# Performance work log

Measured on AMD Instinct MI355X. Metric: run time of the kernel, lower is better.

The kernel has to match this reference:

```python
import math
import jax, jax.numpy as jnp
import numpy as np

B, A, M, NC = 32, 8400, 32, 80
TOP_K, ALPHA, BETA, EPS = 13, 1.0, 6.0, 1e-9
IMG = 640.0


def _ciou(b1, b2, eps=1e-7):
    # b1, b2 broadcastable [..., 4]; CIoU as in compute_iou (box1=gt, box2=pred)
    b1x1, b1y1, b1x2, b1y2 = b1[..., 0], b1[..., 1], b1[..., 2], b1[..., 3]
    b2x1, b2y1, b2x2, b2y2 = b2[..., 0], b2[..., 1], b2[..., 2], b2[..., 3]
    w1, h1 = b1x2 - b1x1, b1y2 - b1y1 + eps
    w2, h2 = b2x2 - b2x1, b2y2 - b2y1 + eps
    inter = (jnp.minimum(b1x2, b2x2) - jnp.maximum(b1x1, b2x1)).clip(0) * \
            (jnp.minimum(b1y2, b2y2) - jnp.maximum(b1y1, b2y1)).clip(0)
    union = w1 * h1 + w2 * h2 - inter + eps
    iou = inter / union
    cw = jnp.maximum(b1x2, b2x2) - jnp.minimum(b1x1, b2x1)
    ch = jnp.maximum(b1y2, b2y2) - jnp.minimum(b1y1, b2y1)
    c2 = cw ** 2 + ch ** 2 + eps
    rho2 = ((b2x1 + b2x2 - b1x1 - b1x2) ** 2 + (b2y1 + b2y2 - b1y1 - b1y2) ** 2) / 4.0
    v = (4.0 / math.pi ** 2) * (jnp.arctan(w2 / h2) - jnp.arctan(w1 / h1)) ** 2
    alpha = jax.lax.stop_gradient(v / (v - iou + (1.0 + eps)))
    return iou - (rho2 / c2 + v * alpha)


def setup_inputs() -> dict:
    key = jax.random.key(0)
    ks = jax.random.split(key, 8)
    pd_scores = jax.random.uniform(ks[0], (B, A, NC), jnp.float32)
    anc_points = jax.random.uniform(ks[1], (A, 2), jnp.float32) * IMG
    # predicted boxes around anchor points (valid x1<x2, y1<y2)
    off = jax.random.uniform(ks[2], (B, A, 4), jnp.float32) * 80.0 + 2.0
    pd_bboxes = jnp.concatenate([anc_points[None] - off[..., :2],
                                 anc_points[None] + off[..., 2:]], -1)
    # GT boxes: random centers and sizes, clipped to image
    c = jax.random.uniform(ks[3], (B, M, 2), jnp.float32) * IMG
    wh = jax.random.uniform(ks[4], (B, M, 2), jnp.float32) * 180.0 + 20.0
    gt_bboxes = jnp.concatenate([(c - wh / 2).clip(0, IMG), (c + wh / 2).clip(0, IMG)], -1)
    gt_labels = jax.random.randint(ks[5], (B, M, 1), 0, NC, jnp.int64)
    n_valid = jax.random.randint(ks[6], (B,), 1, M + 1)
    mask_gt = (jnp.arange(M)[None, :] < n_valid[:, None]).astype(jnp.float32)[..., None]
    return {"pd_scores": pd_scores, "pd_bboxes": pd_bboxes, "anc_points": anc_points,
            "gt_labels": gt_labels, "gt_bboxes": gt_bboxes, "mask_gt": mask_gt}


def reference(pd_scores, pd_bboxes, anc_points, gt_labels, gt_bboxes, mask_gt):
    b, a, nc = pd_scores.shape
    m = gt_bboxes.shape[1]
    dtype = pd_scores.dtype

    # anchors-inside-GT mask: [B,M,A]
    lt = gt_bboxes[:, :, None, :2]          # [B,M,1,2]
    rb = gt_bboxes[:, :, None, 2:]
    deltas = jnp.concatenate([anc_points[None, None] - lt,
                              rb - anc_points[None, None]], -1)  # [B,M,A,4]
    mask_in_gts = deltas.min(-1) > EPS
    mg = mask_gt[..., 0] > 0                 # [B,M] bool
    gt_mask = mask_in_gts & mg[:, :, None]

    # per-GT class score gather: pd_scores[b, :, gt_labels[b,m]] -> [B,M,A]
    labels = gt_labels[..., 0]               # [B,M]
    idx = jnp.broadcast_to(labels[:, :, None, None], (b, m, a, 1))
    gathered = jnp.take_along_axis(jnp.broadcast_to(pd_scores[:, None], (b, m, a, nc)), idx, axis=3)[..., 0]
    bbox_scores = jnp.where(gt_mask, gathered, 0.0)

    # CIoU overlaps (dense, masked) [B,M,A]
    iou = _ciou(gt_bboxes[:, :, None, :], pd_bboxes[:, None, :, :])
    overlaps = jnp.where(gt_mask, jnp.maximum(iou, 0.0), 0.0)

    align_metric = bbox_scores ** ALPHA * overlaps ** BETA

    # top-k selection with duplicate suppression (faithful to scatter_add loop)
    _, tk_idx = jax.lax.top_k(align_metric, TOP_K)      # [B,M,K]
    tk_mask = jnp.broadcast_to(mg[:, :, None], tk_idx.shape)
    tk_idx = jnp.where(tk_mask, tk_idx, 0)
    bi = jnp.arange(b)[:, None, None]
    mi = jnp.arange(m)[None, :, None]
    counts = jnp.zeros((b, m, a), jnp.int32).at[bi, mi, tk_idx].add(1)
    mask_top_k = jnp.where(counts > 1, 0, counts).astype(dtype)

    mask_pos = mask_top_k * mask_in_gts.astype(dtype) * mg[:, :, None].astype(dtype)
    fg_mask = mask_pos.sum(1)                            # [B,A]

    # resolve anchors assigned to multiple GTs (no-op when none; matches torch branch)
    mask_multi = fg_mask[:, None, :] > 1                 # [B,M,A] (broadcast)
    max_idx = overlaps.argmax(1)                         # [B,A]
    is_max = (jnp.arange(m)[None, :, None] == max_idx[:, None, :]).astype(dtype)
    mask_pos = jnp.where(mask_multi, is_max, mask_pos)
    fg_mask = mask_pos.sum(1)

    target_gt_idx = mask_pos.argmax(1)                   # [B,A]
    target_labels = jnp.maximum(jnp.take_along_axis(labels, target_gt_idx, axis=1), 0)
    target_bboxes = jnp.take_along_axis(
        gt_bboxes, jnp.broadcast_to(target_gt_idx[..., None], (b, a, 4)), axis=1)

    target_scores = jax.nn.one_hot(target_labels, NC, dtype=dtype)
    target_scores = jnp.where((fg_mask > 0)[..., None], target_scores, 0.0)

    am = align_metric * mask_pos
    pos_am = am.max(-1, keepdims=True)                   # [B,M,1]
    pos_ov = (overlaps * mask_pos).max(-1, keepdims=True)
    norm = (am * pos_ov / (pos_am + EPS)).max(1)[..., None]  # [B,A,1]
    target_scores = target_scores * norm

    return target_bboxes, target_scores, fg_mask > 0
```

## Files before the change

### kernel.cpp

```cpp
#include <hip/hip_runtime.h>
#include <math.h>

#define BB 32
#define AA 8400
#define MM 32
#define NCC 80
#define TOPK 13
#define CAP 1024
#define NW (AA / 32 + 1)

typedef float nfloat4 __attribute__((ext_vector_type(4)));

__device__ __forceinline__ void wave_argmax(float& v, int& i) {
    #pragma unroll
    for (int off = 32; off > 0; off >>= 1) {
        float ov = __shfl_xor(v, off, 64);
        int oi = __shfl_xor(i, off, 64);
        if (ov > v || (ov == v && oi < i)) { v = ov; i = oi; }
    }
}

__global__ __launch_bounds__(256) void k12_topk(
        const float* __restrict__ pd_scores, const float* __restrict__ pd_bboxes,
        const float* __restrict__ anc, const int* __restrict__ gt_labels,
        const float* __restrict__ gt_bboxes, const float* __restrict__ mask_gt,
        int* __restrict__ sel_idx, float* __restrict__ pos_am, float* __restrict__ pos_ov) {
    __shared__ float lval[CAP];
    __shared__ int   lidx[CAP];
    __shared__ unsigned int bmask[NW];
    __shared__ float wv[4];
    __shared__ int   wi[4];
    __shared__ int   wsum[4];
    __shared__ int   s_p, s_sel;
    const float eps = 1e-7f;
    int bm = blockIdx.x;
    int b = bm >> 5;
    int tid = threadIdx.x;
    int lane = tid & 63;
    int wid = tid >> 6;
    if (tid == 0) pos_am[bm] = 0.f;
    if (tid == 1) pos_ov[bm] = 0.f;
    if (tid == 2) s_p = 0;
    if (tid == 3) s_sel = 0;
    if (tid < 16) sel_idx[bm * 16 + tid] = -1;
    if (!(mask_gt[bm] > 0.f)) return;

    for (int i = tid; i < NW; i += 256) bmask[i] = 0u;
    float4 g = reinterpret_cast<const float4*>(gt_bboxes)[bm];

    const float4* anc4 = reinterpret_cast<const float4*>(anc);
    unsigned long long bits = 0ull;
    int c_t = 0;
    #pragma unroll
    for (int j = 0; j < 17; j++) {
        int e = tid + (j << 8);
        if (e < 4200) {
            float4 an = anc4[e];
            float d0 = fminf(fminf(an.x - g.x, an.y - g.y), fminf(g.z - an.x, g.w - an.y));
            float d1 = fminf(fminf(an.z - g.x, an.w - g.y), fminf(g.z - an.z, g.w - an.w));
            if (d0 > 1e-9f) { bits |= 1ull << (2 * j);     c_t++; }
            if (d1 > 1e-9f) { bits |= 1ull << (2 * j + 1); c_t++; }
        }
    }
    int x = c_t;
    #pragma unroll
    for (int off = 1; off < 64; off <<= 1) {
        int y = __shfl_up(x, off, 64);
        if (lane >= off) x += y;
    }
    if (lane == 63) wsum[wid] = x;
    __syncthreads();
    int base = 0;
    #pragma unroll
    for (int w = 0; w < 4; w++) if (w < wid) base += wsum[w];
    int n_c = min(wsum[0] + wsum[1] + wsum[2] + wsum[3], CAP);
    {
        int o = base + x - c_t;
        unsigned long long mm_ = bits;
        while (mm_) {
            int k = __builtin_ctzll(mm_);
            mm_ &= mm_ - 1ull;
            int i = 2 * tid + 512 * (k >> 1) + (k & 1);
            if (o < CAP) lidx[o] = i;
            o++;
        }
    }
    for (int s = n_c + tid; s < CAP; s += 256) { lval[s] = -1.f; lidx[s] = AA; }
    __syncthreads();

    float w1 = g.z - g.x, h1 = g.w - g.y + eps;
    float atg = atanf(w1 / h1);
    float w1h1 = w1 * h1;
    float sgx = g.x + g.z, sgy = g.y + g.w;
    int lab = gt_labels[bm];
    const float4* pbb = reinterpret_cast<const float4*>(pd_bboxes) + (long)b * AA;
    const float* scp = pd_scores + (long)b * AA * NCC + lab;
    int nit = (n_c + 255) >> 8;
    for (int it = 0; it < nit; it++) {
        int s = (it << 8) + tid;
        bool pos = false;
        if (s < n_c) {
            int i = lidx[s];
            float4 pb = pbb[i];
            float sc = scp[(long)i * NCC];
            float w2 = pb.z - pb.x, h2 = pb.w - pb.y + eps;
            float iw = fmaxf(fminf(g.z, pb.z) - fmaxf(g.x, pb.x), 0.f);
            float ih = fmaxf(fminf(g.w, pb.w) - fmaxf(g.y, pb.y), 0.f);
            float inter = iw * ih;
            float uni = w1h1 + w2 * h2 - inter + eps;
            float iou = inter / uni;
            float cw = fmaxf(g.z, pb.z) - fminf(g.x, pb.x);
            float ch = fmaxf(g.w, pb.w) - fminf(g.y, pb.y);
            float c2 = cw * cw + ch * ch + eps;
            float dx = pb.x + pb.z - sgx, dy = pb.y + pb.w - sgy;
            float rho2 = (dx * dx + dy * dy) * 0.25f;
            float dv = atanf(w2 / h2) - atg;
            float v = 0.4052847345693511f * dv * dv;
            float alpha = v / (v - iou + (1.0f + eps));
            float cv = iou - (rho2 / c2 + v * alpha);
            float ov = fmaxf(cv, 0.f);
            float o2 = ov * ov;
            float val = sc * o2 * o2 * o2;
            pos = val > 0.f;
            lval[s] = pos ? val : -1.f;
            if (pos) atomicOr(&bmask[i >> 5], 1u << (i & 31));
        }
        unsigned long long pm = __ballot(pos);
        if (lane == 0) atomicAdd(&s_p, (int)__popcll(pm));
    }
    __syncthreads();
    int p = s_p;

    if (p >= TOPK) {
        float v0 = lval[tid], v1 = lval[tid + 256], v2 = lval[tid + 512], v3 = lval[tid + 768];
        int   i0 = lidx[tid], i1 = lidx[tid + 256], i2 = lidx[tid + 512], i3 = lidx[tid + 768];
        int mysel = -1;
        for (int k = 0; k < TOPK; k++) {
            float bv = v0; int bi = i0;
            if (v1 > bv || (v1 == bv && i1 < bi)) { bv = v1; bi = i1; }
            if (v2 > bv || (v2 == bv && i2 < bi)) { bv = v2; bi = i2; }
            if (v3 > bv || (v3 == bv && i3 < bi)) { bv = v3; bi = i3; }
            wave_argmax(bv, bi);
            if (lane == 0) { wv[wid] = bv; wi[wid] = bi; }
            __syncthreads();
            float gv = wv[0]; int gi = wi[0];
            #pragma unroll
            for (int w = 1; w < 4; w++) {
                float ov = wv[w]; int oi = wi[w];
                if (ov > gv || (ov == gv && oi < gi)) { gv = ov; gi = oi; }
            }
            if (tid == k) mysel = gi;
            if (i0 == gi) v0 = -1.f;
            if (i1 == gi) v1 = -1.f;
            if (i2 == gi) v2 = -1.f;
            if (i3 == gi) v3 = -1.f;
            __syncthreads();
        }
        if (tid < TOPK) sel_idx[bm * 16 + tid] = mysel;
    } else {
        for (int s = tid; s < n_c; s += 256)
            if (lval[s] > 0.f) {
                int slot = atomicAdd(&s_sel, 1);
                sel_idx[bm * 16 + slot] = lidx[s];
            }
        if (wid == 0) {
            int need = TOPK - p;
            for (int base_i = 0; need > 0 && base_i < AA; base_i += 64) {
                int i = base_i + lane;
                bool cand = (i < AA) && !((bmask[i >> 5] >> (i & 31)) & 1u);
                unsigned long long wm = __ballot(cand);
                int take = min(need, (int)__popcll(wm));
                if (cand && (int)__popcll(wm & ((1ull << lane) - 1ull)) < take) {
                    float2 an = reinterpret_cast<const float2*>(anc)[i];
                    float dmin = fminf(fminf(an.x - g.x, an.y - g.y), fminf(g.z - an.x, g.w - an.y));
                    if (dmin > 1e-9f) {
                        int slot = atomicAdd(&s_sel, 1);
                        sel_idx[bm * 16 + slot] = i;
                    }
                }
                need -= take;
            }
        }
    }
}

__global__ __launch_bounds__(256) void k3_resolve(
        const float* __restrict__ pd_scores, const float* __restrict__ pd_bboxes,
        const float* __restrict__ anc, const int* __restrict__ gt_labels,
        const float* __restrict__ gt_bboxes, const float* __restrict__ mask_gt,
        const int* __restrict__ sel_idx,
        float* __restrict__ pos_am, float* __restrict__ pos_ov,
        float* __restrict__ out_bbox, float* __restrict__ out_fg,
        int2* __restrict__ meta) {
    __shared__ float sg[MM][8];
    __shared__ int slab[MM];
    __shared__ int smg[MM];
    __shared__ unsigned int selcol[256];
    const float eps = 1e-7f;
    int b = blockIdx.y;
    int tid = threadIdx.x;
    if (tid < MM) {
        int gm = b * MM + tid;
        float4 g = reinterpret_cast<const float4*>(gt_bboxes)[gm];
        float w1 = g.z - g.x, h1 = g.w - g.y + eps;
        sg[tid][0] = g.x; sg[tid][1] = g.y; sg[tid][2] = g.z; sg[tid][3] = g.w;
        sg[tid][4] = w1 * h1;
        sg[tid][5] = atanf(w1 / h1);
        sg[tid][6] = g.x + g.z;
        sg[tid][7] = g.y + g.w;
        int lb = gt_labels[gm]; if (lb < 0) lb = 0;
        slab[tid] = lb;
        smg[tid] = mask_gt[gm] > 0.f ? 1 : 0;
    }
    selcol[tid] = 0u;
    __syncthreads();
    int a0 = blockIdx.x * 256;
    const int* sl = sel_idx + b * MM * 16;
    #pragma unroll
    for (int t = tid; t < MM * 16; t += 256) {
        int e = sl[t];
        if (e >= a0 && e < a0 + 256) atomicOr(&selcol[e - a0], 1u << (t >> 4));
    }
    __syncthreads();
    int a = a0 + tid;
    if (a >= AA) return;
    int g = b * AA + a;
    unsigned int sel = selcol[tid];
    int fg = __popc(sel);

    int tg = 0; bool fgo = false; float ovt = 0.f;
    if (fg >= 1) {
        float ax = anc[a * 2], ay = anc[a * 2 + 1];
        float4 pb = reinterpret_cast<const float4*>(pd_bboxes)[g];
        float w2 = pb.z - pb.x, h2 = pb.w - pb.y + eps;
        float atp = atanf(w2 / h2);
        float w2h2 = w2 * h2;
        float spx = pb.x + pb.z, spy = pb.y + pb.w;
        fgo = true;
        if (fg == 1) {
            tg = __ffs(sel) - 1;
            float gx1 = sg[tg][0], gy1 = sg[tg][1], gx2 = sg[tg][2], gy2 = sg[tg][3];
            float iw = fmaxf(fminf(gx2, pb.z) - fmaxf(gx1, pb.x), 0.f);
            float ih = fmaxf(fminf(gy2, pb.w) - fmaxf(gy1, pb.y), 0.f);
            float inter = iw * ih;
            float uni = sg[tg][4] + w2h2 - inter + eps;
            float iou = inter / uni;
            float cw = fmaxf(gx2, pb.z) - fminf(gx1, pb.x);
            float ch = fmaxf(gy2, pb.w) - fminf(gy1, pb.y);
            float c2 = cw * cw + ch * ch + eps;
            float dx = spx - sg[tg][6], dy = spy - sg[tg][7];
            float rho2 = (dx * dx + dy * dy) * 0.25f;
            float dv = atp - sg[tg][5];
            float v = 0.4052847345693511f * dv * dv;
            float alpha = v / (v - iou + (1.0f + eps));
            ovt = fmaxf(iou - (rho2 / c2 + v * alpha), 0.f);
        } else {
            float bestov = -1.f; int bestm = 0;
            for (int mm = 0; mm < MM; mm++) {
                float gx1 = sg[mm][0], gy1 = sg[mm][1], gx2 = sg[mm][2], gy2 = sg[mm][3];
                float dmin = fminf(fminf(ax - gx1, ay - gy1), fminf(gx2 - ax, gy2 - ay));
                float ov = 0.f;
                if ((dmin > 1e-9f) && smg[mm]) {
                    float iw = fmaxf(fminf(gx2, pb.z) - fmaxf(gx1, pb.x), 0.f);
                    float ih = fmaxf(fminf(gy2, pb.w) - fmaxf(gy1, pb.y), 0.f);
                    float inter = iw * ih;
                    float uni = sg[mm][4] + w2h2 - inter + eps;
                    float iou = inter / uni;
                    float cw = fmaxf(gx2, pb.z) - fminf(gx1, pb.x);
                    float ch = fmaxf(gy2, pb.w) - fminf(gy1, pb.y);
                    float c2 = cw * cw + ch * ch + eps;
                    float dx = spx - sg[mm][6], dy = spy - sg[mm][7];
                    float rho2 = (dx * dx + dy * dy) * 0.25f;
                    float dv = atp - sg[mm][5];
                    float v = 0.4052847345693511f * dv * dv;
                    float alpha = v / (v - iou + (1.0f + eps));
                    ov = fmaxf(iou - (rho2 / c2 + v * alpha), 0.f);
                }
                if (ov > bestov) { bestov = ov; bestm = mm; }
            }
            tg = bestm; ovt = bestov;
        }
    }

    nfloat4 gb = {sg[tg][0], sg[tg][1], sg[tg][2], sg[tg][3]};
    __builtin_nontemporal_store(gb, reinterpret_cast<nfloat4*>(out_bbox) + g);
    out_fg[g] = fgo ? 1.f : 0.f;
    float amv = 0.f;
    if (fgo) {
        float sc = pd_scores[(long)g * NCC + slab[tg]];
        float o2 = ovt * ovt;
        amv = sc * o2 * o2 * o2;
        atomicMax((int*)&pos_am[b * MM + tg], __float_as_int(amv));
        atomicMax((int*)&pos_ov[b * MM + tg], __float_as_int(ovt));
    }
    meta[g] = make_int2(__float_as_int(amv), tg | (slab[tg] << 8) | ((fgo ? 1 : 0) << 16));
}

__global__ __launch_bounds__(256) void k4_scores(
        const int2* __restrict__ meta,
        const float* __restrict__ pos_am, const float* __restrict__ pos_ov,
        float* __restrict__ out_scores) {
    int g = blockIdx.x * 256 + threadIdx.x;
    const int NQ = NCC / 4;
    if (g >= BB * AA * NQ) return;
    int ba = g / NQ;
    int c0 = (g % NQ) * 4;
    nfloat4 o = {0.f, 0.f, 0.f, 0.f};
    int2 mt = meta[ba];
    int p = mt.y;
    if (p & (1 << 16)) {
        int tg = p & 31, lab = (p >> 8) & 127;
        int b = ba / AA;
        int bm = b * MM + tg;
        float nv = (__int_as_float(mt.x) * pos_ov[bm]) / (pos_am[bm] + 1e-9f);
        int d = lab - c0;
        if (d == 0) o.x = nv; else if (d == 1) o.y = nv;
        else if (d == 2) o.z = nv; else if (d == 3) o.w = nv;
    }
    __builtin_nontemporal_store(o, reinterpret_cast<nfloat4*>(out_scores) + g);
}

extern "C" void kernel_launch(void* const* d_in, const int* in_sizes, int n_in,
                              void* d_out, int out_size, void* d_ws, size_t ws_size,
                              hipStream_t stream) {
    const float* pd_scores = (const float*)d_in[0];
    const float* pd_bboxes = (const float*)d_in[1];
    const float* anc       = (const float*)d_in[2];
    const int*   gt_labels = (const int*)d_in[3];
    const float* gt_bboxes = (const float*)d_in[4];
    const float* mask_gt   = (const float*)d_in[5];

    const long nBA = (long)BB * AA;

    char* ws = (char*)d_ws;
    int*   sel_idx = (int*)ws;                  ws += (long)BB * MM * 16 * 4;
    float* pos_am  = (float*)ws;                ws += BB * MM * 4;
    float* pos_ov  = (float*)ws;                ws += BB * MM * 4;
    int2*  meta    = (int2*)ws;                 ws += nBA * 8;

    float* out_bbox   = (float*)d_out;
    float* out_scores = out_bbox + nBA * 4;
    float* out_fg     = out_scores + nBA * NCC;

    k12_topk<<<BB * MM, 256, 0, stream>>>(pd_scores, pd_bboxes, anc, gt_labels,
                                          gt_bboxes, mask_gt, sel_idx, pos_am, pos_ov);
    dim3 g3((AA + 255) / 256, BB);
    k3_resolve<<<g3, 256, 0, stream>>>(pd_scores, pd_bboxes, anc, gt_labels,
                                       gt_bboxes, mask_gt, sel_idx, pos_am, pos_ov,
                                       out_bbox, out_fg, meta);
    long nS4 = nBA * (NCC / 4);
    k4_scores<<<(int)((nS4 + 255) / 256), 256, 0, stream>>>(meta, pos_am, pos_ov, out_scores);
}
```

Measured before the change: 187.6 us.

## Widen top-k kernel to 1024 threads, one candidate per thread

The per-GT top-k kernel now launches 1024 threads per block instead of 256. Each thread handles one candidate slot, so the CIoU loop and the 4-way register preselection in the top-k selection go away, and the anchor scan uses fewer iterations. The cross-wave reduction now spans 16 waves, and each of the 13 selection rounds pays for a larger block-wide barrier. Large blocks may also lower occupancy when many blocks exit early or have few candidates.

```diff
diff --git a/kernel.cpp b/kernel.cpp
--- a/kernel.cpp
+++ b/kernel.cpp
@@ -8,6 +8,7 @@
 #define TOPK 13
 #define CAP 1024
 #define NW (AA / 32 + 1)
+#define K12T 1024
 
 typedef float nfloat4 __attribute__((ext_vector_type(4)));
 
@@ -20,7 +21,7 @@
     }
 }
 
-__global__ __launch_bounds__(256) void k12_topk(
+__global__ __launch_bounds__(K12T) void k12_topk(
         const float* __restrict__ pd_scores, const float* __restrict__ pd_bboxes,
         const float* __restrict__ anc, const int* __restrict__ gt_labels,
         const float* __restrict__ gt_bboxes, const float* __restrict__ mask_gt,
@@ -28,9 +29,9 @@
     __shared__ float lval[CAP];
     __shared__ int   lidx[CAP];
     __shared__ unsigned int bmask[NW];
-    __shared__ float wv[4];
-    __shared__ int   wi[4];
-    __shared__ int   wsum[4];
+    __shared__ float wv[16];
+    __shared__ int   wi[16];
+    __shared__ int   wsum[16];
     __shared__ int   s_p, s_sel;
     const float eps = 1e-7f;
     int bm = blockIdx.x;
@@ -45,21 +46,21 @@
     if (tid < 16) sel_idx[bm * 16 + tid] = -1;
     if (!(mask_gt[bm] > 0.f)) return;
 
-    for (int i = tid; i < NW; i += 256) bmask[i] = 0u;
+    for (int i = tid; i < NW; i += K12T) bmask[i] = 0u;
     float4 g = reinterpret_cast<const float4*>(gt_bboxes)[bm];
 
     const float4* anc4 = reinterpret_cast<const float4*>(anc);
-    unsigned long long bits = 0ull;
+    unsigned int bits = 0u;
     int c_t = 0;
     #pragma unroll
-    for (int j = 0; j < 17; j++) {
-        int e = tid + (j << 8);
+    for (int j = 0; j < 5; j++) {
+        int e = tid + (j << 10);
         if (e < 4200) {
             float4 an = anc4[e];
             float d0 = fminf(fminf(an.x - g.x, an.y - g.y), fminf(g.z - an.x, g.w - an.y));
             float d1 = fminf(fminf(an.z - g.x, an.w - g.y), fminf(g.z - an.z, g.w - an.w));
-            if (d0 > 1e-9f) { bits |= 1ull << (2 * j);     c_t++; }
-            if (d1 > 1e-9f) { bits |= 1ull << (2 * j + 1); c_t++; }
+            if (d0 > 1e-9f) { bits |= 1u << (2 * j);     c_t++; }
+            if (d1 > 1e-9f) { bits |= 1u << (2 * j + 1); c_t++; }
         }
     }
     int x = c_t;
@@ -70,22 +71,22 @@
     }
     if (lane == 63) wsum[wid] = x;
     __syncthreads();
-    int base = 0;
-    #pragma unroll
-    for (int w = 0; w < 4; w++) if (w < wid) base += wsum[w];
-    int n_c = min(wsum[0] + wsum[1] + wsum[2] + wsum[3], CAP);
+    int base = 0, tot = 0;
+    #pragma unroll
+    for (int w = 0; w < 16; w++) { int s = wsum[w]; if (w < wid) base += s; tot += s; }
+    int n_c = min(tot, CAP);
     {
         int o = base + x - c_t;
-        unsigned long long mm_ = bits;
+        unsigned int mm_ = bits;
         while (mm_) {
-            int k = __builtin_ctzll(mm_);
-            mm_ &= mm_ - 1ull;
-            int i = 2 * tid + 512 * (k >> 1) + (k & 1);
+            int k = __builtin_ctz(mm_);
+            mm_ &= mm_ - 1u;
+            int i = 2 * tid + ((k >> 1) << 11) + (k & 1);
             if (o < CAP) lidx[o] = i;
             o++;
         }
     }
-    for (int s = n_c + tid; s < CAP; s += 256) { lval[s] = -1.f; lidx[s] = AA; }
+    for (int s = n_c + tid; s < CAP; s += K12T) { lval[s] = -1.f; lidx[s] = AA; }
     __syncthreads();
 
     float w1 = g.z - g.x, h1 = g.w - g.y + eps;
@@ -95,9 +96,8 @@
     int lab = gt_labels[bm];
     const float4* pbb = reinterpret_cast<const float4*>(pd_bboxes) + (long)b * AA;
     const float* scp = pd_scores + (long)b * AA * NCC + lab;
-    int nit = (n_c + 255) >> 8;
-    for (int it = 0; it < nit; it++) {
-        int s = (it << 8) + tid;
+    {
+        int s = tid;
         bool pos = false;
         if (s < n_c) {
             int i = lidx[s];
@@ -132,37 +132,30 @@
     int p = s_p;
 
     if (p >= TOPK) {
-        float v0 = lval[tid], v1 = lval[tid + 256], v2 = lval[tid + 512], v3 = lval[tid + 768];
-        int   i0 = lidx[tid], i1 = lidx[tid + 256], i2 = lidx[tid + 512], i3 = lidx[tid + 768];
+        float v0 = lval[tid];
+        int   i0 = lidx[tid];
         int mysel = -1;
         for (int k = 0; k < TOPK; k++) {
             float bv = v0; int bi = i0;
-            if (v1 > bv || (v1 == bv && i1 < bi)) { bv = v1; bi = i1; }
-            if (v2 > bv || (v2 == bv && i2 < bi)) { bv = v2; bi = i2; }
-            if (v3 > bv || (v3 == bv && i3 < bi)) { bv = v3; bi = i3; }
             wave_argmax(bv, bi);
             if (lane == 0) { wv[wid] = bv; wi[wid] = bi; }
             __syncthreads();
             float gv = wv[0]; int gi = wi[0];
             #pragma unroll
-            for (int w = 1; w < 4; w++) {
+            for (int w = 1; w < 16; w++) {
                 float ov = wv[w]; int oi = wi[w];
                 if (ov > gv || (ov == gv && oi < gi)) { gv = ov; gi = oi; }
             }
             if (tid == k) mysel = gi;
             if (i0 == gi) v0 = -1.f;
-            if (i1 == gi) v1 = -1.f;
-            if (i2 == gi) v2 = -1.f;
-            if (i3 == gi) v3 = -1.f;
             __syncthreads();
         }
         if (tid < TOPK) sel_idx[bm * 16 + tid] = mysel;
     } else {
-        for (int s = tid; s < n_c; s += 256)
-            if (lval[s] > 0.f) {
-                int slot = atomicAdd(&s_sel, 1);
-                sel_idx[bm * 16 + slot] = lidx[s];
-            }
+        if (tid < n_c && lval[tid] > 0.f) {
+            int slot = atomicAdd(&s_sel, 1);
+            sel_idx[bm * 16 + slot] = lidx[tid];
+        }
         if (wid == 0) {
             int need = TOPK - p;
             for (int base_i = 0; need > 0 && base_i < AA; base_i += 64) {
@@ -342,8 +335,8 @@
     float* out_scores = out_bbox + nBA * 4;
     float* out_fg     = out_scores + nBA * NCC;
 
-    k12_topk<<<BB * MM, 256, 0, stream>>>(pd_scores, pd_bboxes, anc, gt_labels,
-                                          gt_bboxes, mask_gt, sel_idx, pos_am, pos_ov);
+    k12_topk<<<BB * MM, K12T, 0, stream>>>(pd_scores, pd_bboxes, anc, gt_labels,
+                                           gt_bboxes, mask_gt, sel_idx, pos_am, pos_ov);
     dim3 g3((AA + 255) / 256, BB);
     k3_resolve<<<g3, 256, 0, stream>>>(pd_scores, pd_bboxes, anc, gt_labels,
                                        gt_bboxes, mask_gt, sel_idx, pos_am, pos_ov,
```

New measurement: 231.3 us. 23.3% more time.

## Split candidate scoring into anchor-tiled kernel with global candidate lists

Applied to the files above, without the earlier changes.

Replaces the per-GT block kernel, which scanned all anchors and gathered scores and boxes for every GT, with an anchor-tiled kernel. That kernel stages a tile of scores and predicted boxes in shared memory and evaluates all 32 GTs against it, appending positive candidates to per-GT global lists through atomics. A separate top-k kernel then reads those lists. The aim is coalesced score loads and reuse of predicted-box data across GTs, at the cost of two extra launches, global atomics and nondeterministic candidate order, which may change tie-breaking.

```diff
diff --git a/kernel.cpp b/kernel.cpp
--- a/kernel.cpp
+++ b/kernel.cpp
@@ -7,7 +7,8 @@
 #define NCC 80
 #define TOPK 13
 #define CAP 1024
-#define NW (AA / 32 + 1)
+#define TILE 128
+#define NTILE ((AA + TILE - 1) / TILE)
 
 typedef float nfloat4 __attribute__((ext_vector_type(4)));
 
@@ -20,120 +21,126 @@
     }
 }
 
-__global__ __launch_bounds__(256) void k12_topk(
+__global__ __launch_bounds__(256) void k0_zero(int* __restrict__ gcnt) {
+    int t = threadIdx.x;
+    #pragma unroll
+    for (int j = 0; j < 4; j++) gcnt[t + j * 256] = 0;
+}
+
+__global__ __launch_bounds__(256) void k1_cand(
         const float* __restrict__ pd_scores, const float* __restrict__ pd_bboxes,
         const float* __restrict__ anc, const int* __restrict__ gt_labels,
         const float* __restrict__ gt_bboxes, const float* __restrict__ mask_gt,
+        int* __restrict__ gcnt, int2* __restrict__ cand) {
+    __shared__ float  ssc[TILE * NCC];
+    __shared__ float4 spb[TILE];
+    __shared__ float  sax[TILE], say[TILE], satp[TILE], sw2h2[TILE], sspx[TILE], sspy[TILE];
+    __shared__ float  sg[MM][8];
+    __shared__ int    slab[MM], smg[MM];
+    const float eps = 1e-7f;
+    int b  = blockIdx.y;
+    int a0 = blockIdx.x * TILE;
+    int na = min(TILE, AA - a0);
+    int tid = threadIdx.x;
+
+    const float4* s4 = reinterpret_cast<const float4*>(pd_scores + ((long)b * AA + a0) * NCC);
+    int nq = na * (NCC / 4);
+    for (int j = tid; j < nq; j += 256) reinterpret_cast<float4*>(ssc)[j] = s4[j];
+    if (tid < na) {
+        float4 pb = reinterpret_cast<const float4*>(pd_bboxes)[(long)b * AA + a0 + tid];
+        spb[tid] = pb;
+        float2 an = reinterpret_cast<const float2*>(anc)[a0 + tid];
+        sax[tid] = an.x; say[tid] = an.y;
+        float w2 = pb.z - pb.x, h2 = pb.w - pb.y + eps;
+        satp[tid]  = atanf(w2 / h2);
+        sw2h2[tid] = w2 * h2;
+        sspx[tid]  = pb.x + pb.z;
+        sspy[tid]  = pb.y + pb.w;
+    }
+    if (tid >= 128 && tid < 128 + MM) {
+        int m = tid - 128;
+        int gm = b * MM + m;
+        float4 g = reinterpret_cast<const float4*>(gt_bboxes)[gm];
+        float w1 = g.z - g.x, h1 = g.w - g.y + eps;
+        sg[m][0] = g.x; sg[m][1] = g.y; sg[m][2] = g.z; sg[m][3] = g.w;
+        sg[m][4] = w1 * h1;
+        sg[m][5] = atanf(w1 / h1);
+        sg[m][6] = g.x + g.z;
+        sg[m][7] = g.y + g.w;
+        slab[m] = gt_labels[gm];
+        smg[m]  = mask_gt[gm] > 0.f ? 1 : 0;
+    }
+    __syncthreads();
+
+    int npair = na * MM;
+    for (int pr = tid; pr < npair; pr += 256) {
+        int al = pr >> 5;
+        int m  = pr & 31;
+        if (!smg[m]) continue;
+        float ax = sax[al], ay = say[al];
+        float gx1 = sg[m][0], gy1 = sg[m][1], gx2 = sg[m][2], gy2 = sg[m][3];
+        float dmin = fminf(fminf(ax - gx1, ay - gy1), fminf(gx2 - ax, gy2 - ay));
+        if (dmin > 1e-9f) {
+            float4 pb = spb[al];
+            float iw = fmaxf(fminf(gx2, pb.z) - fmaxf(gx1, pb.x), 0.f);
+            float ih = fmaxf(fminf(gy2, pb.w) - fmaxf(gy1, pb.y), 0.f);
+            float inter = iw * ih;
+            float uni = sg[m][4] + sw2h2[al] - inter + eps;
+            float iou = inter / uni;
+            float cw = fmaxf(gx2, pb.z) - fminf(gx1, pb.x);
+            float ch = fmaxf(gy2, pb.w) - fminf(gy1, pb.y);
+            float c2 = cw * cw + ch * ch + eps;
+            float dx = sspx[al] - sg[m][6], dy = sspy[al] - sg[m][7];
+            float rho2 = (dx * dx + dy * dy) * 0.25f;
+            float dv = satp[al] - sg[m][5];
+            float v = 0.4052847345693511f * dv * dv;
+            float alpha = v / (v - iou + (1.0f + eps));
+            float cv = iou - (rho2 / c2 + v * alpha);
+            float ov = fmaxf(cv, 0.f);
+            if (ov > 0.f) {
+                float sc = ssc[al * NCC + slab[m]];
+                float o2 = ov * ov;
+                float val = sc * o2 * o2 * o2;
+                if (val > 0.f) {
+                    int bm = b * MM + m;
+                    int slot = atomicAdd(&gcnt[bm], 1);
+                    if (slot < CAP) cand[(long)bm * CAP + slot] = make_int2(__float_as_int(val), a0 + al);
+                }
+            }
+        }
+    }
+}
+
+__global__ __launch_bounds__(256) void k2b_topk(
+        const int2* __restrict__ cand, const int* __restrict__ gcnt,
+        const float* __restrict__ anc, const float* __restrict__ gt_bboxes,
+        const float* __restrict__ mask_gt,
         int* __restrict__ sel_idx, float* __restrict__ pos_am, float* __restrict__ pos_ov) {
-    __shared__ float lval[CAP];
-    __shared__ int   lidx[CAP];
-    __shared__ unsigned int bmask[NW];
     __shared__ float wv[4];
     __shared__ int   wi[4];
-    __shared__ int   wsum[4];
-    __shared__ int   s_p, s_sel;
-    const float eps = 1e-7f;
+    __shared__ int   pos_idx[16];
+    __shared__ int   s_sel;
     int bm = blockIdx.x;
-    int b = bm >> 5;
     int tid = threadIdx.x;
     int lane = tid & 63;
     int wid = tid >> 6;
     if (tid == 0) pos_am[bm] = 0.f;
     if (tid == 1) pos_ov[bm] = 0.f;
-    if (tid == 2) s_p = 0;
-    if (tid == 3) s_sel = 0;
     if (tid < 16) sel_idx[bm * 16 + tid] = -1;
     if (!(mask_gt[bm] > 0.f)) return;
 
-    for (int i = tid; i < NW; i += 256) bmask[i] = 0u;
-    float4 g = reinterpret_cast<const float4*>(gt_bboxes)[bm];
-
-    const float4* anc4 = reinterpret_cast<const float4*>(anc);
-    unsigned long long bits = 0ull;
-    int c_t = 0;
-    #pragma unroll
-    for (int j = 0; j < 17; j++) {
-        int e = tid + (j << 8);
-        if (e < 4200) {
-            float4 an = anc4[e];
-            float d0 = fminf(fminf(an.x - g.x, an.y - g.y), fminf(g.z - an.x, g.w - an.y));
-            float d1 = fminf(fminf(an.z - g.x, an.w - g.y), fminf(g.z - an.z, g.w - an.w));
-            if (d0 > 1e-9f) { bits |= 1ull << (2 * j);     c_t++; }
-            if (d1 > 1e-9f) { bits |= 1ull << (2 * j + 1); c_t++; }
-        }
-    }
-    int x = c_t;
-    #pragma unroll
-    for (int off = 1; off < 64; off <<= 1) {
-        int y = __shfl_up(x, off, 64);
-        if (lane >= off) x += y;
-    }
-    if (lane == 63) wsum[wid] = x;
-    __syncthreads();
-    int base = 0;
-    #pragma unroll
-    for (int w = 0; w < 4; w++) if (w < wid) base += wsum[w];
-    int n_c = min(wsum[0] + wsum[1] + wsum[2] + wsum[3], CAP);
-    {
-        int o = base + x - c_t;
-        unsigned long long mm_ = bits;
-        while (mm_) {
-            int k = __builtin_ctzll(mm_);
-            mm_ &= mm_ - 1ull;
-            int i = 2 * tid + 512 * (k >> 1) + (k & 1);
-            if (o < CAP) lidx[o] = i;
-            o++;
-        }
-    }
-    for (int s = n_c + tid; s < CAP; s += 256) { lval[s] = -1.f; lidx[s] = AA; }
-    __syncthreads();
-
-    float w1 = g.z - g.x, h1 = g.w - g.y + eps;
-    float atg = atanf(w1 / h1);
-    float w1h1 = w1 * h1;
-    float sgx = g.x + g.z, sgy = g.y + g.w;
-    int lab = gt_labels[bm];
-    const float4* pbb = reinterpret_cast<const float4*>(pd_bboxes) + (long)b * AA;
-    const float* scp = pd_scores + (long)b * AA * NCC + lab;
-    int nit = (n_c + 255) >> 8;
-    for (int it = 0; it < nit; it++) {
-        int s = (it << 8) + tid;
-        bool pos = false;
-        if (s < n_c) {
-            int i = lidx[s];
-            float4 pb = pbb[i];
-            float sc = scp[(long)i * NCC];
-            float w2 = pb.z - pb.x, h2 = pb.w - pb.y + eps;
-            float iw = fmaxf(fminf(g.z, pb.z) - fmaxf(g.x, pb.x), 0.f);
-            float ih = fmaxf(fminf(g.w, pb.w) - fmaxf(g.y, pb.y), 0.f);
-            float inter = iw * ih;
-            float uni = w1h1 + w2 * h2 - inter + eps;
-            float iou = inter / uni;
-            float cw = fmaxf(g.z, pb.z) - fminf(g.x, pb.x);
-            float ch = fmaxf(g.w, pb.w) - fminf(g.y, pb.y);
-            float c2 = cw * cw + ch * ch + eps;
-            float dx = pb.x + pb.z - sgx, dy = pb.y + pb.w - sgy;
-            float rho2 = (dx * dx + dy * dy) * 0.25f;
-            float dv = atanf(w2 / h2) - atg;
-            float v = 0.4052847345693511f * dv * dv;
-            float alpha = v / (v - iou + (1.0f + eps));
-            float cv = iou - (rho2 / c2 + v * alpha);
-            float ov = fmaxf(cv, 0.f);
-            float o2 = ov * ov;
-            float val = sc * o2 * o2 * o2;
-            pos = val > 0.f;
-            lval[s] = pos ? val : -1.f;
-            if (pos) atomicOr(&bmask[i >> 5], 1u << (i & 31));
-        }
-        unsigned long long pm = __ballot(pos);
-        if (lane == 0) atomicAdd(&s_p, (int)__popcll(pm));
-    }
-    __syncthreads();
-    int p = s_p;
-
-    if (p >= TOPK) {
-        float v0 = lval[tid], v1 = lval[tid + 256], v2 = lval[tid + 512], v3 = lval[tid + 768];
-        int   i0 = lidx[tid], i1 = lidx[tid + 256], i2 = lidx[tid + 512], i3 = lidx[tid + 768];
+    int n = min(gcnt[bm], CAP);
+    const int2* cb = cand + (long)bm * CAP;
+
+    if (n >= TOPK) {
+        float v0, v1, v2, v3; int i0, i1, i2, i3;
+        {
+            int s;
+            s = tid;       if (s < n) { int2 c = cb[s]; v0 = __int_as_float(c.x); i0 = c.y; } else { v0 = -1.f; i0 = AA; }
+            s = tid + 256; if (s < n) { int2 c = cb[s]; v1 = __int_as_float(c.x); i1 = c.y; } else { v1 = -1.f; i1 = AA; }
+            s = tid + 512; if (s < n) { int2 c = cb[s]; v2 = __int_as_float(c.x); i2 = c.y; } else { v2 = -1.f; i2 = AA; }
+            s = tid + 768; if (s < n) { int2 c = cb[s]; v3 = __int_as_float(c.x); i3 = c.y; } else { v3 = -1.f; i3 = AA; }
+        }
         int mysel = -1;
         for (int k = 0; k < TOPK; k++) {
             float bv = v0; int bi = i0;
@@ -158,19 +165,19 @@
         }
         if (tid < TOPK) sel_idx[bm * 16 + tid] = mysel;
     } else {
-        for (int s = tid; s < n_c; s += 256)
-            if (lval[s] > 0.f) {
-                int slot = atomicAdd(&s_sel, 1);
-                sel_idx[bm * 16 + slot] = lidx[s];
-            }
+        if (tid == 0) s_sel = n;
+        if (tid < n) { int2 c = cb[tid]; sel_idx[bm * 16 + tid] = c.y; pos_idx[tid] = c.y; }
+        __syncthreads();
         if (wid == 0) {
-            int need = TOPK - p;
+            float4 g = reinterpret_cast<const float4*>(gt_bboxes)[bm];
+            int need = TOPK - n;
             for (int base_i = 0; need > 0 && base_i < AA; base_i += 64) {
                 int i = base_i + lane;
-                bool cand = (i < AA) && !((bmask[i >> 5] >> (i & 31)) & 1u);
-                unsigned long long wm = __ballot(cand);
+                bool candl = (i < AA);
+                for (int q = 0; q < n; q++) if (i == pos_idx[q]) candl = false;
+                unsigned long long wm = __ballot(candl);
                 int take = min(need, (int)__popcll(wm));
-                if (cand && (int)__popcll(wm & ((1ull << lane) - 1ull)) < take) {
+                if (candl && (int)__popcll(wm & ((1ull << lane) - 1ull)) < take) {
                     float2 an = reinterpret_cast<const float2*>(anc)[i];
                     float dmin = fminf(fminf(an.x - g.x, an.y - g.y), fminf(g.z - an.x, g.w - an.y));
                     if (dmin > 1e-9f) {
@@ -331,19 +338,26 @@
     const float* mask_gt   = (const float*)d_in[5];
 
     const long nBA = (long)BB * AA;
+    const long nBM = (long)BB * MM;
 
     char* ws = (char*)d_ws;
-    int*   sel_idx = (int*)ws;                  ws += (long)BB * MM * 16 * 4;
-    float* pos_am  = (float*)ws;                ws += BB * MM * 4;
-    float* pos_ov  = (float*)ws;                ws += BB * MM * 4;
+    int2*  cand    = (int2*)ws;                 ws += nBM * CAP * 8;
     int2*  meta    = (int2*)ws;                 ws += nBA * 8;
+    int*   gcnt    = (int*)ws;                  ws += nBM * 4;
+    int*   sel_idx = (int*)ws;                  ws += nBM * 16 * 4;
+    float* pos_am  = (float*)ws;                ws += nBM * 4;
+    float* pos_ov  = (float*)ws;                ws += nBM * 4;
 
     float* out_bbox   = (float*)d_out;
     float* out_scores = out_bbox + nBA * 4;
     float* out_fg     = out_scores + nBA * NCC;
 
-    k12_topk<<<BB * MM, 256, 0, stream>>>(pd_scores, pd_bboxes, anc, gt_labels,
-                                          gt_bboxes, mask_gt, sel_idx, pos_am, pos_ov);
+    k0_zero<<<1, 256, 0, stream>>>(gcnt);
+    dim3 g1(NTILE, BB);
+    k1_cand<<<g1, 256, 0, stream>>>(pd_scores, pd_bboxes, anc, gt_labels,
+                                    gt_bboxes, mask_gt, gcnt, cand);
+    k2b_topk<<<(int)nBM, 256, 0, stream>>>(cand, gcnt, anc, gt_bboxes, mask_gt,
+                                           sel_idx, pos_am, pos_ov);
     dim3 g3((AA + 255) / 256, BB);
     k3_resolve<<<g3, 256, 0, stream>>>(pd_scores, pd_bboxes, anc, gt_labels,
                                        gt_bboxes, mask_gt, sel_idx, pos_am, pos_ov,
```

Result: slower. 283.6 us (+51.2%).
